# Kernel tuning notes

Hardware: AMD Instinct MI355X
Metric: run time of the kernel (lower is better)

Reference implementation:

```python
import jax, jax.numpy as jnp
import numpy as np

N, B, D = 2048, 4, 2048   # seq_len, batch, embed_dim (sequence-first layout)
E = 2                     # expand_ratio
H = D // E                # number of heads
EPS = 1e-5


def setup_inputs() -> dict:
    key = jax.random.key(0)
    ks = jax.random.split(key, 3)
    x = jax.random.normal(ks[0], (N, B, D), dtype=jnp.float32)
    W_in = jax.random.normal(ks[1], (3 * D, D), dtype=jnp.float32) / np.sqrt(D).astype(np.float32)
    b_in = jnp.zeros((3 * D,), jnp.float32)
    W_out = jax.random.normal(ks[2], (D, D), dtype=jnp.float32) / np.sqrt(D).astype(np.float32)
    b_out = jnp.zeros((D,), jnp.float32)
    gamma = jnp.ones((D,), jnp.float32)
    beta = jnp.zeros((D,), jnp.float32)
    return {"x": x, "W_in": W_in, "b_in": b_in, "gamma": gamma, "beta": beta,
            "W_out": W_out, "b_out": b_out}


def _linear_scan(lam, u):
    # h_t = lam_t * h_{t-1} + u_t along time axis 0 (HgruRealFunction)
    def combine(c1, c2):
        a1, b1 = c1
        a2, b2 = c2
        return a1 * a2, a2 * b1 + b2
    _, h = jax.lax.associative_scan(combine, (lam, u), axis=0)
    return h


def _layernorm(x, gamma, beta):
    mu = jnp.mean(x, axis=-1, keepdims=True)
    var = jnp.var(x, axis=-1, keepdims=True)
    return (x - mu) * jax.lax.rsqrt(var + EPS) * gamma + beta


def reference(x, W_in, b_in, gamma, beta, W_out, b_out):
    n, b, d = x.shape
    feat = x @ W_in.T + b_in                       # (n,b,3d)
    inp, og, fg = jnp.split(feat, 3, axis=-1)
    inp = jax.nn.silu(inp)                         # act_fun = silu
    og = jax.nn.sigmoid(og)                        # uv_act_fun = sigmoid
    lam = jax.nn.sigmoid(fg)                       # lower_bound = 0 => lambda = sigmoid(F)

    inp = inp.reshape(n, b, H, E)
    og = og.reshape(n, b, H, E)
    lam = lam.reshape(n, b, H, E)

    # input = einsum('...hd,...he->...hde', 1-lambda, input)
    u = ((1.0 - lam)[..., :, None] * inp[..., None, :]).reshape(n, b, H * E * E)
    lam_f = jnp.broadcast_to(lam[..., :, None], (n, b, H, E, E)).reshape(n, b, H * E * E)

    s_fwd = _linear_scan(lam_f, u)
    s_rev = jnp.flip(_linear_scan(jnp.flip(lam_f, 0), jnp.flip(u, 0)), 0)
    s = (s_fwd + s_rev).reshape(n, b, H, E, E)

    o = jnp.einsum('nbhde,nbhd->nbhe', s, og).reshape(n, b, d)
    o = _layernorm(o, gamma, beta)
    return o @ W_out.T + b_out
```

## Files before the change

kernel.cpp:

```cpp
#include <hip/hip_runtime.h>
#include <hip/hip_bf16.h>

#define NSEQ 2048
#define NB   4
#define DIM  2048
#define HN   1024
#define FC   6144
#define MROWS 8192
#define CHUNKS 64
#define CLEN 32
#define NCH  4096

typedef __bf16 bf16x8_t __attribute__((ext_vector_type(8)));
typedef float  f32x4_t  __attribute__((ext_vector_type(4)));

__device__ __forceinline__ float sigm(float x){ return 1.f/(1.f + __expf(-x)); }
__device__ __forceinline__ float bflo(unsigned p){ return __uint_as_float(p << 16); }
__device__ __forceinline__ float bfhi(unsigned p){ return __uint_as_float(p & 0xffff0000u); }
__device__ __forceinline__ unsigned short f2bf(float f){
  union { __hip_bfloat16 h; unsigned short u; } cv;
  cv.h = __float2bfloat16(f);
  return cv.u;
}

__global__ __launch_bounds__(256) void cvt_bf16_4(const float4* __restrict__ in,
                                                  ushort4* __restrict__ out, int n4){
  int i = blockIdx.x * blockDim.x + threadIdx.x;
  int st = gridDim.x * blockDim.x;
  for (; i < n4; i += st){
    float4 v = in[i];
    ushort4 r;
    r.x = f2bf(v.x); r.y = f2bf(v.y); r.z = f2bf(v.z); r.w = f2bf(v.w);
    out[i] = r;
  }
}

__device__ __forceinline__ void gl_lds16(const void* g, void* l){
  __builtin_amdgcn_global_load_lds((const __attribute__((address_space(1))) void*)g,
                                   (__attribute__((address_space(3))) void*)l, 16, 0, 0);
}

template <typename OutT>
__global__ __launch_bounds__(512, 2) void gemm256(const __hip_bfloat16* __restrict__ A,
                                                  const __hip_bfloat16* __restrict__ B,
                                                  const float* __restrict__ bias,
                                                  OutT* __restrict__ C,
                                                  int M, int N, int K, int nbx){
  __shared__ __align__(16) __hip_bfloat16 smem[4*16384];
  const int tid  = threadIdx.x;
  const int wave = tid >> 6, lane = tid & 63;

  const int cpx = gridDim.x >> 3;
  const int wg  = (blockIdx.x & 7) * cpx + (blockIdx.x >> 3);
  const int bx = wg % nbx, by = wg / nbx;
  const int m0 = by * 256, n0 = bx * 256;

  const int wr = wave >> 2, wc = wave & 3;
  const int r  = lane & 15, q = lane >> 4;
  const int kx = q ^ (r & 7);

  int goffA[4], goffB[4], ldso[4];
  #pragma unroll
  for (int i = 0; i < 4; ++i){
    int g = i*512 + tid;
    int row = g >> 3;
    int k16 = (g & 7) ^ (row & 7);
    goffA[i] = (m0 + row) * K + k16*8;
    goffB[i] = (n0 + row) * K + k16*8;
    ldso[i]  = g * 8;
  }
  auto stage = [&](int kt, int bufo){
    #pragma unroll
    for (int i = 0; i < 4; ++i){
      gl_lds16(A + goffA[i] + kt, smem + bufo + ldso[i]);
      gl_lds16(B + goffB[i] + kt, smem + bufo + 16384 + ldso[i]);
    }
  };

  const int arow = wr*128 + r;
  const int brow = wc*64  + r;

  f32x4_t acc[8][4] = {};

  const int NT = K >> 6;
  stage(0, 0);
  __syncthreads();
  int curo = 0;

  for (int t = 0; t < NT; ++t){
    if (t + 1 < NT) stage((t+1)*64, curo ^ 32768);
    #pragma unroll
    for (int ksub = 0; ksub < 2; ++ksub){
      const int kphys = (kx ^ (ksub << 2)) << 3;
      const __hip_bfloat16* Ab = smem + curo + arow*64 + kphys;
      const __hip_bfloat16* Bb = smem + curo + 16384 + brow*64 + kphys;
      bf16x8_t bfr[4];
      #pragma unroll
      for (int fn = 0; fn < 4; ++fn)
        bfr[fn] = *reinterpret_cast<const bf16x8_t*>(Bb + fn*1024);
      #pragma unroll
      for (int half = 0; half < 2; ++half){
        bf16x8_t af[4];
        #pragma unroll
        for (int i = 0; i < 4; ++i)
          af[i] = *reinterpret_cast<const bf16x8_t*>(Ab + (half*4 + i)*1024);
        __builtin_amdgcn_s_setprio(1);
        #pragma unroll
        for (int i = 0; i < 4; ++i)
          #pragma unroll
          for (int fn = 0; fn < 4; ++fn)
            acc[half*4 + i][fn] =
              __builtin_amdgcn_mfma_f32_16x16x32_bf16(af[i], bfr[fn], acc[half*4 + i][fn], 0, 0, 0);
        __builtin_amdgcn_s_setprio(0);
      }
    }
    __syncthreads();
    curo ^= 32768;
  }

  #pragma unroll
  for (int fn = 0; fn < 4; ++fn){
    int col = n0 + wc*64 + fn*16 + r;
    float bv = bias[col];
    #pragma unroll
    for (int fm = 0; fm < 8; ++fm){
      int row0 = m0 + wr*128 + fm*16 + q*4;
      #pragma unroll
      for (int j = 0; j < 4; ++j){
        float v = acc[fm][fn][j] + bv;
        if constexpr (__is_same(OutT, float))
          C[(size_t)(row0 + j)*N + col] = v;
        else
          C[(size_t)(row0 + j)*N + col] = __float2bfloat16(v);
      }
    }
  }
}

struct SV { float l0, l1, u00, u01, u10, u11; };
__device__ __forceinline__ SV stepv(const unsigned* __restrict__ fp, int rowu){
  unsigned pi = fp[rowu];
  unsigned pf = fp[rowu + 2048];
  SV s;
  s.l0 = sigm(bflo(pf)); s.l1 = sigm(bfhi(pf));
  float i0 = bflo(pi), i1 = bfhi(pi);
  i0 *= sigm(i0); i1 *= sigm(i1);
  float a0 = 1.f - s.l0, a1 = 1.f - s.l1;
  s.u00 = a0*i0; s.u01 = a0*i1; s.u10 = a1*i0; s.u11 = a1*i1;
  return s;
}

__global__ __launch_bounds__(256) void scan_agg(const unsigned* __restrict__ feat,
    float* __restrict__ aggP, float4* __restrict__ aggHF, float4* __restrict__ aggHR){
  int ch = blockIdx.x*256 + threadIdx.x;
  int c  = blockIdx.y;
  int b = ch >> 10, h = ch & 1023;
  int base = b*3072 + h;
  int n0 = c*CLEN;
  float P0 = 1.f, P1 = 1.f;
  float f00=0,f01=0,f10=0,f11=0;
  for (int t = 0; t < CLEN; ++t){
    SV s = stepv(feat, (n0+t)*12288 + base);
    f00 = s.l0*f00 + s.u00; f01 = s.l0*f01 + s.u01;
    f10 = s.l1*f10 + s.u10; f11 = s.l1*f11 + s.u11;
    P0 *= s.l0; P1 *= s.l1;
  }
  float r00=0,r01=0,r10=0,r11=0;
  for (int t = CLEN-1; t >= 0; --t){
    SV s = stepv(feat, (n0+t)*12288 + base);
    r00 = s.l0*r00 + s.u00; r01 = s.l0*r01 + s.u01;
    r10 = s.l1*r10 + s.u10; r11 = s.l1*r11 + s.u11;
  }
  aggP[c*8192 + ch*2]     = P0;
  aggP[c*8192 + ch*2 + 1] = P1;
  aggHF[c*4096 + ch] = make_float4(f00,f01,f10,f11);
  aggHR[c*4096 + ch] = make_float4(r00,r01,r10,r11);
}

__global__ __launch_bounds__(256) void scan_carry(const float* __restrict__ aggP,
    const float* __restrict__ aggHF, const float* __restrict__ aggHR,
    float* __restrict__ cF, float* __restrict__ cR){
  int t  = blockIdx.x*256 + threadIdx.x;
  int pd = t >> 1;
  float s = 0.f;
  for (int c = 0; c < CHUNKS; ++c){
    cF[c*16384 + t] = s;
    s = aggP[c*8192 + pd]*s + aggHF[c*16384 + t];
  }
  s = 0.f;
  for (int c = CHUNKS-1; c >= 0; --c){
    cR[c*16384 + t] = s;
    s = aggP[c*8192 + pd]*s + aggHR[c*16384 + t];
  }
}

__global__ __launch_bounds__(256) void scan_fwd(const unsigned* __restrict__ feat,
    const float4* __restrict__ cF, float2* __restrict__ o){
  int ch = blockIdx.x*256 + threadIdx.x;
  int c  = blockIdx.y;
  int b = ch >> 10, h = ch & 1023;
  int base = b*3072 + h;
  float4 hv = cF[c*4096 + ch];
  float h00=hv.x, h01=hv.y, h10=hv.z, h11=hv.w;
  for (int t = 0; t < CLEN; ++t){
    int n = c*CLEN + t;
    int rowu = n*12288 + base;
    SV s = stepv(feat, rowu);
    h00 = s.l0*h00 + s.u00; h01 = s.l0*h01 + s.u01;
    h10 = s.l1*h10 + s.u10; h11 = s.l1*h11 + s.u11;
    unsigned po = feat[rowu + 1024];
    float g0 = sigm(bflo(po)), g1 = sigm(bfhi(po));
    o[(n*NB + b)*1024 + h] = make_float2(g0*h00 + g1*h10, g0*h01 + g1*h11);
  }
}

__global__ __launch_bounds__(256) void scan_rev(const unsigned* __restrict__ feat,
    const float4* __restrict__ cR, float2* __restrict__ o){
  int ch = blockIdx.x*256 + threadIdx.x;
  int c  = blockIdx.y;
  int b = ch >> 10, h = ch & 1023;
  int base = b*3072 + h;
  float4 hv = cR[c*4096 + ch];
  float h00=hv.x, h01=hv.y, h10=hv.z, h11=hv.w;
  for (int t = CLEN-1; t >= 0; --t){
    int n = c*CLEN + t;
    int rowu = n*12288 + base;
    SV s = stepv(feat, rowu);
    h00 = s.l0*h00 + s.u00; h01 = s.l0*h01 + s.u01;
    h10 = s.l1*h10 + s.u10; h11 = s.l1*h11 + s.u11;
    unsigned po = feat[rowu + 1024];
    float g0 = sigm(bflo(po)), g1 = sigm(bfhi(po));
    int idx = (n*NB + b)*1024 + h;
    float2 pv = o[idx];
    o[idx] = make_float2(pv.x + g0*h00 + g1*h10, pv.y + g0*h01 + g1*h11);
  }
}

__global__ __launch_bounds__(256) void layernorm_k(const float* __restrict__ o,
    const float* __restrict__ gamma, const float* __restrict__ beta,
    __hip_bfloat16* __restrict__ out){
  int row = blockIdx.x, t = threadIdx.x;
  const float4* x = (const float4*)(o + (size_t)row*DIM);
  float4 a = x[t], b = x[t + 256];
  float s  = (a.x + a.y) + (a.z + a.w) + (b.x + b.y) + (b.z + b.w);
  float ss = (a.x*a.x + a.y*a.y) + (a.z*a.z + a.w*a.w)
           + (b.x*b.x + b.y*b.y) + (b.z*b.z + b.w*b.w);
  #pragma unroll
  for (int off = 32; off > 0; off >>= 1){
    s  += __shfl_down(s, off);
    ss += __shfl_down(ss, off);
  }
  __shared__ float red[8];
  int wv = t >> 6, ln = t & 63;
  if (ln == 0){ red[wv] = s; red[4 + wv] = ss; }
  __syncthreads();
  float S  = (red[0] + red[1]) + (red[2] + red[3]);
  float SS = (red[4] + red[5]) + (red[6] + red[7]);
  float mu = S * (1.f/DIM);
  float rs = rsqrtf(SS * (1.f/DIM) - mu*mu + 1e-5f);
  const float4* gp = (const float4*)gamma;
  const float4* bp = (const float4*)beta;
  float4 g0 = gp[t], g1 = gp[t + 256], be0 = bp[t], be1 = bp[t + 256];
  ushort4* op = (ushort4*)(out + (size_t)row*DIM);
  ushort4 r0, r1;
  r0.x = f2bf((a.x - mu)*rs*g0.x + be0.x);
  r0.y = f2bf((a.y - mu)*rs*g0.y + be0.y);
  r0.z = f2bf((a.z - mu)*rs*g0.z + be0.z);
  r0.w = f2bf((a.w - mu)*rs*g0.w + be0.w);
  r1.x = f2bf((b.x - mu)*rs*g1.x + be1.x);
  r1.y = f2bf((b.y - mu)*rs*g1.y + be1.y);
  r1.z = f2bf((b.z - mu)*rs*g1.z + be1.z);
  r1.w = f2bf((b.w - mu)*rs*g1.w + be1.w);
  op[t] = r0; op[t + 256] = r1;
}

extern "C" void kernel_launch(void* const* d_in, const int* in_sizes, int n_in,
                              void* d_out, int out_size, void* d_ws, size_t ws_size,
                              hipStream_t stream){
  (void)in_sizes; (void)n_in; (void)out_size;
  const float* x     = (const float*)d_in[0];
  const float* W_in  = (const float*)d_in[1];
  const float* b_in  = (const float*)d_in[2];
  const float* gamma = (const float*)d_in[3];
  const float* beta  = (const float*)d_in[4];
  const float* W_out = (const float*)d_in[5];
  const float* b_out = (const float*)d_in[6];
  float* out = (float*)d_out;

  char* p = (char*)d_ws;
  auto carve = [&](size_t bytes) -> char* {
    char* r = p; p += (bytes + 255) & ~(size_t)255; return r;
  };
  __hip_bfloat16* feat = (__hip_bfloat16*)carve((size_t)MROWS*FC*2);
  char* U              = carve((size_t)MROWS*DIM*4);
  __hip_bfloat16* Wob  = (__hip_bfloat16*)carve((size_t)DIM*DIM*2);
  float* aggP  = (float*)carve((size_t)CHUNKS*8192*4);
  float* aggHF = (float*)carve((size_t)CHUNKS*16384*4);
  float* aggHR = (float*)carve((size_t)CHUNKS*16384*4);
  float* cF    = (float*)carve((size_t)CHUNKS*16384*4);
  float* cR    = (float*)carve((size_t)CHUNKS*16384*4);
  if ((size_t)(p - (char*)d_ws) > ws_size) return;

  __hip_bfloat16* xb  = (__hip_bfloat16*)U;
  __hip_bfloat16* Wib = (__hip_bfloat16*)(U + (size_t)MROWS*DIM*2);
  float* o            = (float*)U;
  __hip_bfloat16* oln = (__hip_bfloat16*)feat;

  cvt_bf16_4<<<2048, 256, 0, stream>>>((const float4*)x,     (ushort4*)xb,  MROWS*DIM/4);
  cvt_bf16_4<<<2048, 256, 0, stream>>>((const float4*)W_in,  (ushort4*)Wib, FC*DIM/4);
  cvt_bf16_4<<<1024, 256, 0, stream>>>((const float4*)W_out, (ushort4*)Wob, DIM*DIM/4);

  gemm256<__hip_bfloat16><<<768, 512, 0, stream>>>(xb, Wib, b_in, feat, MROWS, FC, 2048, FC/256);

  scan_agg  <<<dim3(NCH/256, CHUNKS), 256, 0, stream>>>((const unsigned*)feat, aggP, (float4*)aggHF, (float4*)aggHR);
  scan_carry<<<64, 256, 0, stream>>>(aggP, aggHF, aggHR, cF, cR);
  scan_fwd  <<<dim3(NCH/256, CHUNKS), 256, 0, stream>>>((const unsigned*)feat, (const float4*)cF, (float2*)o);
  scan_rev  <<<dim3(NCH/256, CHUNKS), 256, 0, stream>>>((const unsigned*)feat, (const float4*)cR, (float2*)o);

  layernorm_k<<<MROWS, 256, 0, stream>>>(o, gamma, beta, oln);

  gemm256<float><<<256, 512, 0, stream>>>(oln, Wob, b_out, out, MROWS, DIM, 2048, DIM/256);
}
```

Baseline: 440.4 us.

## Triple-buffer GEMM with register prefetch and fuse forward/reverse scan kernels

The GEMM moves from a double-buffered 64-wide K tile to a triple-buffered 32-wide K tile. Loads run two stages ahead, and the next tile's fragments are prefetched into registers while the current MFMAs run. LDS use drops and the barrier count per K doubles. Separately, the forward and reverse chunk scans are merged into one kernel that holds the 32 per-step outputs in registers and writes o once, which removes the read-modify-write of o and one launch at the cost of higher register pressure.

```diff
diff --git a/kernel.cpp b/kernel.cpp
--- a/kernel.cpp
+++ b/kernel.cpp
@@ -46,7 +46,7 @@
                                                   const float* __restrict__ bias,
                                                   OutT* __restrict__ C,
                                                   int M, int N, int K, int nbx){
-  __shared__ __align__(16) __hip_bfloat16 smem[4*16384];
+  __shared__ __align__(16) __hip_bfloat16 smem[3*16384];
   const int tid  = threadIdx.x;
   const int wave = tid >> 6, lane = tid & 63;
 
@@ -57,65 +57,55 @@
 
   const int wr = wave >> 2, wc = wave & 3;
   const int r  = lane & 15, q = lane >> 4;
-  const int kx = q ^ (r & 7);
-
-  int goffA[4], goffB[4], ldso[4];
-  #pragma unroll
-  for (int i = 0; i < 4; ++i){
-    int g = i*512 + tid;
-    int row = g >> 3;
-    int k16 = (g & 7) ^ (row & 7);
-    goffA[i] = (m0 + row) * K + k16*8;
-    goffB[i] = (n0 + row) * K + k16*8;
-    ldso[i]  = g * 8;
-  }
-  auto stage = [&](int kt, int bufo){
-    #pragma unroll
-    for (int i = 0; i < 4; ++i){
-      gl_lds16(A + goffA[i] + kt, smem + bufo + ldso[i]);
-      gl_lds16(B + goffB[i] + kt, smem + bufo + 16384 + ldso[i]);
+  const int kph = (q ^ (r & 3)) * 8;
+
+  auto stage = [&](int kt, int bo){
+    #pragma unroll
+    for (int i = 0; i < 2; ++i){
+      int g = i*512 + tid;
+      int row = g >> 2;
+      int k16 = (g & 3) ^ (row & 3);
+      gl_lds16(A + (size_t)(m0 + row)*K + kt + k16*8, smem + bo + g*8);
+      gl_lds16(B + (size_t)(n0 + row)*K + kt + k16*8, smem + bo + 8192 + g*8);
     }
   };
-
-  const int arow = wr*128 + r;
-  const int brow = wc*64  + r;
+  const int arow = (wr*128 + r) * 32 + kph;
+  const int brow = 8192 + (wc*64 + r) * 32 + kph;
 
   f32x4_t acc[8][4] = {};
-
-  const int NT = K >> 6;
+  const int NT = K >> 5;
+
   stage(0, 0);
+  stage(32, 16384);
   __syncthreads();
-  int curo = 0;
+
+  bf16x8_t Fa[8], Fb[4];
+  #pragma unroll
+  for (int i = 0; i < 8; ++i) Fa[i] = *reinterpret_cast<const bf16x8_t*>(smem + arow + i*512);
+  #pragma unroll
+  for (int j = 0; j < 4; ++j) Fb[j] = *reinterpret_cast<const bf16x8_t*>(smem + brow + j*512);
 
   for (int t = 0; t < NT; ++t){
-    if (t + 1 < NT) stage((t+1)*64, curo ^ 32768);
-    #pragma unroll
-    for (int ksub = 0; ksub < 2; ++ksub){
-      const int kphys = (kx ^ (ksub << 2)) << 3;
-      const __hip_bfloat16* Ab = smem + curo + arow*64 + kphys;
-      const __hip_bfloat16* Bb = smem + curo + 16384 + brow*64 + kphys;
-      bf16x8_t bfr[4];
+    int b2 = 16384 * ((t+2) % 3);
+    if (t + 2 < NT) stage((t+2)*32, b2);
+    int rb = (t+1 < NT) ? 16384*((t+1)%3) : 16384*(t%3);
+    bf16x8_t Na[8], Nb[4];
+    #pragma unroll
+    for (int j = 0; j < 4; ++j) Nb[j] = *reinterpret_cast<const bf16x8_t*>(smem + rb + brow + j*512);
+    #pragma unroll
+    for (int i = 0; i < 8; ++i) Na[i] = *reinterpret_cast<const bf16x8_t*>(smem + rb + arow + i*512);
+    __builtin_amdgcn_s_setprio(1);
+    #pragma unroll
+    for (int i = 0; i < 8; ++i)
       #pragma unroll
-      for (int fn = 0; fn < 4; ++fn)
-        bfr[fn] = *reinterpret_cast<const bf16x8_t*>(Bb + fn*1024);
-      #pragma unroll
-      for (int half = 0; half < 2; ++half){
-        bf16x8_t af[4];
-        #pragma unroll
-        for (int i = 0; i < 4; ++i)
-          af[i] = *reinterpret_cast<const bf16x8_t*>(Ab + (half*4 + i)*1024);
-        __builtin_amdgcn_s_setprio(1);
-        #pragma unroll
-        for (int i = 0; i < 4; ++i)
-          #pragma unroll
-          for (int fn = 0; fn < 4; ++fn)
-            acc[half*4 + i][fn] =
-              __builtin_amdgcn_mfma_f32_16x16x32_bf16(af[i], bfr[fn], acc[half*4 + i][fn], 0, 0, 0);
-        __builtin_amdgcn_s_setprio(0);
-      }
-    }
+      for (int j = 0; j < 4; ++j)
+        acc[i][j] = __builtin_amdgcn_mfma_f32_16x16x32_bf16(Fa[i], Fb[j], acc[i][j], 0, 0, 0);
+    __builtin_amdgcn_s_setprio(0);
     __syncthreads();
-    curo ^= 32768;
+    #pragma unroll
+    for (int i = 0; i < 8; ++i) Fa[i] = Na[i];
+    #pragma unroll
+    for (int j = 0; j < 4; ++j) Fb[j] = Nb[j];
   }
 
   #pragma unroll
@@ -194,46 +184,46 @@
   }
 }
 
-__global__ __launch_bounds__(256) void scan_fwd(const unsigned* __restrict__ feat,
-    const float4* __restrict__ cF, float2* __restrict__ o){
+__global__ __launch_bounds__(256) void scan_fr(const unsigned* __restrict__ feat,
+    const float4* __restrict__ cF, const float4* __restrict__ cR,
+    float2* __restrict__ o){
   int ch = blockIdx.x*256 + threadIdx.x;
   int c  = blockIdx.y;
   int b = ch >> 10, h = ch & 1023;
   int base = b*3072 + h;
-  float4 hv = cF[c*4096 + ch];
-  float h00=hv.x, h01=hv.y, h10=hv.z, h11=hv.w;
-  for (int t = 0; t < CLEN; ++t){
-    int n = c*CLEN + t;
-    int rowu = n*12288 + base;
-    SV s = stepv(feat, rowu);
-    h00 = s.l0*h00 + s.u00; h01 = s.l0*h01 + s.u01;
-    h10 = s.l1*h10 + s.u10; h11 = s.l1*h11 + s.u11;
-    unsigned po = feat[rowu + 1024];
-    float g0 = sigm(bflo(po)), g1 = sigm(bfhi(po));
-    o[(n*NB + b)*1024 + h] = make_float2(g0*h00 + g1*h10, g0*h01 + g1*h11);
-  }
-}
-
-__global__ __launch_bounds__(256) void scan_rev(const unsigned* __restrict__ feat,
-    const float4* __restrict__ cR, float2* __restrict__ o){
-  int ch = blockIdx.x*256 + threadIdx.x;
-  int c  = blockIdx.y;
-  int b = ch >> 10, h = ch & 1023;
-  int base = b*3072 + h;
-  float4 hv = cR[c*4096 + ch];
-  float h00=hv.x, h01=hv.y, h10=hv.z, h11=hv.w;
-  for (int t = CLEN-1; t >= 0; --t){
-    int n = c*CLEN + t;
-    int rowu = n*12288 + base;
-    SV s = stepv(feat, rowu);
-    h00 = s.l0*h00 + s.u00; h01 = s.l0*h01 + s.u01;
-    h10 = s.l1*h10 + s.u10; h11 = s.l1*h11 + s.u11;
-    unsigned po = feat[rowu + 1024];
-    float g0 = sigm(bflo(po)), g1 = sigm(bfhi(po));
-    int idx = (n*NB + b)*1024 + h;
-    float2 pv = o[idx];
-    o[idx] = make_float2(pv.x + g0*h00 + g1*h10, pv.y + g0*h01 + g1*h11);
-  }
+  float2 accv[CLEN];
+  {
+    float4 hv = cF[c*4096 + ch];
+    float h00=hv.x, h01=hv.y, h10=hv.z, h11=hv.w;
+    #pragma unroll
+    for (int t = 0; t < CLEN; ++t){
+      int rowu = (c*CLEN + t)*12288 + base;
+      SV s = stepv(feat, rowu);
+      h00 = s.l0*h00 + s.u00; h01 = s.l0*h01 + s.u01;
+      h10 = s.l1*h10 + s.u10; h11 = s.l1*h11 + s.u11;
+      unsigned po = feat[rowu + 1024];
+      float g0 = sigm(bflo(po)), g1 = sigm(bfhi(po));
+      accv[t] = make_float2(g0*h00 + g1*h10, g0*h01 + g1*h11);
+    }
+  }
+  {
+    float4 hv = cR[c*4096 + ch];
+    float h00=hv.x, h01=hv.y, h10=hv.z, h11=hv.w;
+    #pragma unroll
+    for (int t = CLEN-1; t >= 0; --t){
+      int rowu = (c*CLEN + t)*12288 + base;
+      SV s = stepv(feat, rowu);
+      h00 = s.l0*h00 + s.u00; h01 = s.l0*h01 + s.u01;
+      h10 = s.l1*h10 + s.u10; h11 = s.l1*h11 + s.u11;
+      unsigned po = feat[rowu + 1024];
+      float g0 = sigm(bflo(po)), g1 = sigm(bfhi(po));
+      accv[t].x += g0*h00 + g1*h10;
+      accv[t].y += g0*h01 + g1*h11;
+    }
+  }
+  #pragma unroll
+  for (int t = 0; t < CLEN; ++t)
+    o[((c*CLEN + t)*NB + b)*1024 + h] = accv[t];
 }
 
 __global__ __launch_bounds__(256) void layernorm_k(const float* __restrict__ o,
@@ -314,8 +304,7 @@
 
   scan_agg  <<<dim3(NCH/256, CHUNKS), 256, 0, stream>>>((const unsigned*)feat, aggP, (float4*)aggHF, (float4*)aggHR);
   scan_carry<<<64, 256, 0, stream>>>(aggP, aggHF, aggHR, cF, cR);
-  scan_fwd  <<<dim3(NCH/256, CHUNKS), 256, 0, stream>>>((const unsigned*)feat, (const float4*)cF, (float2*)o);
-  scan_rev  <<<dim3(NCH/256, CHUNKS), 256, 0, stream>>>((const unsigned*)feat, (const float4*)cR, (float2*)o);
+  scan_fr   <<<dim3(NCH/256, CHUNKS), 256, 0, stream>>>((const unsigned*)feat, (const float4*)cF, (const float4*)cR, (float2*)o);
 
   layernorm_k<<<MROWS, 256, 0, stream>>>(o, gamma, beta, oln);
 
```

After: 496.5 us. +12.7%, slower.
